# Performance work log

Hardware: AMD Instinct MI355X
Metric: run time of the kernel (lower is better)

Reference implementation:

```python
import jax, jax.numpy as jnp
import numpy as np

N = 50000
E = 800000
D_IN = 128
D_OUT = 64


def setup_inputs() -> dict:
    key = jax.random.key(0)
    ks = jax.random.split(key, 8)
    x = jax.random.normal(ks[0], (N, D_IN), dtype=jnp.float32)
    edge_index = jax.random.randint(ks[1], (2, E), 0, N, dtype=jnp.int64)
    s = 1.0 / np.sqrt(D_IN)
    # PyG SAGEConv: lin_l (applied to aggregated neighbors, has bias), lin_r (root, no bias)
    w1_l = jax.random.uniform(ks[2], (D_IN, D_IN), jnp.float32, -s, s)
    b1 = jnp.zeros((D_IN,), jnp.float32)
    w1_r = jax.random.uniform(ks[3], (D_IN, D_IN), jnp.float32, -s, s)
    w2_l = jax.random.uniform(ks[4], (D_IN, D_OUT), jnp.float32, -s, s)
    b2 = jnp.zeros((D_OUT,), jnp.float32)
    w2_r = jax.random.uniform(ks[5], (D_IN, D_OUT), jnp.float32, -s, s)
    return {"x": x, "edge_index": edge_index, "w1_l": w1_l, "b1": b1,
            "w1_r": w1_r, "w2_l": w2_l, "b2": b2, "w2_r": w2_r}


def _sage_conv(x, src, dst, w_l, b_l, w_r):
    # mean-aggregate source features at destination nodes
    msg_sum = jax.ops.segment_sum(x[src], dst, num_segments=N)  # [N, d]
    cnt = jax.ops.segment_sum(jnp.ones((src.shape[0],), x.dtype), dst, num_segments=N)
    mean = msg_sum / jnp.maximum(cnt, 1.0)[:, None]
    out = mean @ w_l + b_l + x @ w_r
    # L2 normalize (normalize=True)
    norm = jnp.linalg.norm(out, axis=-1, keepdims=True)
    return out / jnp.maximum(norm, 1e-12)


def reference(x, edge_index, w1_l, b1, w1_r, w2_l, b2, w2_r):
    src, dst = edge_index[0], edge_index[1]
    h = _sage_conv(x, src, dst, w1_l, b1, w1_r)
    h = _sage_conv(h, src, dst, w2_l, b2, w2_r)
    return h
```

## Files before the change

### kernel.cpp

```cpp
#include <hip/hip_runtime.h>
#include <math.h>

#define NN 50000
#define EE 800000
#define NB 196
#define CAP 6144

typedef __attribute__((ext_vector_type(8))) short bf16x8;
typedef __attribute__((ext_vector_type(16))) float f32x16;
typedef __attribute__((ext_vector_type(4))) unsigned short us4;

__device__ inline unsigned short bf16_rne(float f) {
    union { float f; unsigned u; } a; a.f = f;
    unsigned u = a.u;
    u += 0x7fff + ((u >> 16) & 1);
    return (unsigned short)(u >> 16);
}
__device__ inline float bf16_to_f32(unsigned short u) {
    union { unsigned u; float f; } a; a.u = ((unsigned)u) << 16;
    return a.f;
}

__global__ __launch_bounds__(1024) void bin_kernel(
        const int* __restrict__ src, const int* __restrict__ dst,
        int* __restrict__ gcur, int* __restrict__ rec, int E) {
    __shared__ int hist[NB];
    __shared__ int cur[NB];
    const int t = threadIdx.x;
    const int per = (E + gridDim.x - 1) / gridDim.x;
    const int lo = blockIdx.x * per;
    const int hi = min(lo + per, E);

    for (int i = t; i < NB; i += 1024) hist[i] = 0;
    __syncthreads();
    for (int e = lo + t; e < hi; e += 1024)
        atomicAdd(&hist[dst[e] >> 8], 1);
    __syncthreads();
    for (int i = t; i < NB; i += 1024)
        cur[i] = atomicAdd(&gcur[i], hist[i]);
    __syncthreads();
    for (int e = lo + t; e < hi; e += 1024) {
        int d = dst[e], s = src[e];
        int cb = d >> 8;
        int p = atomicAdd(&cur[cb], 1);
        if (p < CAP) rec[(size_t)cb * CAP + p] = ((d & 255) << 16) | s;
    }
}

__global__ __launch_bounds__(256) void bucket_deg_kernel(
        const int* __restrict__ rec, const int* __restrict__ bcur,
        int* __restrict__ deg, int n) {
    __shared__ int cnt[256];
    const int cb = blockIdx.x, t = threadIdx.x;
    cnt[t] = 0;
    __syncthreads();
    int m = bcur[cb]; if (m > CAP) m = CAP;
    const int* r = rec + (size_t)cb * CAP;
    for (int i = t; i < m; i += 256) atomicAdd(&cnt[r[i] >> 16], 1);
    __syncthreads();
    int node = cb * 256 + t;
    if (node < n) deg[node] = cnt[t];
}

__global__ void scan1_kernel(const int* __restrict__ deg, int* __restrict__ bsum, int n) {
    __shared__ int s[256];
    int t = threadIdx.x;
    int i = blockIdx.x * 256 + t;
    s[t] = (i < n) ? deg[i] : 0;
    __syncthreads();
    for (int ofs = 128; ofs > 0; ofs >>= 1) {
        if (t < ofs) s[t] += s[t + ofs];
        __syncthreads();
    }
    if (t == 0) bsum[blockIdx.x] = s[0];
}

__global__ void scan2_kernel(int* __restrict__ bsum, int nb) {
    __shared__ int s[256];
    int t = threadIdx.x;
    s[t] = (t < nb) ? bsum[t] : 0;
    __syncthreads();
    for (int ofs = 1; ofs < 256; ofs <<= 1) {
        int v = s[t];
        int a = (t >= ofs) ? s[t - ofs] : 0;
        __syncthreads();
        s[t] = v + a;
        __syncthreads();
    }
    if (t < nb) bsum[t] = (t == 0) ? 0 : s[t - 1];
}

__global__ void scan3_kernel(const int* __restrict__ deg, const int* __restrict__ bsum,
                             int* __restrict__ rowoff, int n) {
    __shared__ int s[256];
    int t = threadIdx.x;
    int i = blockIdx.x * 256 + t;
    int d = (i < n) ? deg[i] : 0;
    s[t] = d;
    __syncthreads();
    for (int ofs = 1; ofs < 256; ofs <<= 1) {
        int v = s[t];
        int a = (t >= ofs) ? s[t - ofs] : 0;
        __syncthreads();
        s[t] = v + a;
        __syncthreads();
    }
    int excl = s[t] - d + bsum[blockIdx.x];
    if (i < n) rowoff[i] = excl;
    if (i == n - 1) rowoff[n] = excl + d;
}

__global__ __launch_bounds__(256) void place_kernel(
        const int* __restrict__ rec, const int* __restrict__ bcur,
        const int* __restrict__ rowoff, unsigned short* __restrict__ csr, int n) {
    __shared__ int cnt[256];
    __shared__ int cur[256];
    __shared__ unsigned short sorted[CAP];
    const int cb = blockIdx.x, t = threadIdx.x;
    int m = bcur[cb]; if (m > CAP) m = CAP;
    const int* r = rec + (size_t)cb * CAP;

    cnt[t] = 0;
    __syncthreads();
    for (int i = t; i < m; i += 256) atomicAdd(&cnt[r[i] >> 16], 1);
    __syncthreads();
    int orig = cnt[t];
    for (int ofs = 1; ofs < 256; ofs <<= 1) {
        int v = cnt[t];
        int a = (t >= ofs) ? cnt[t - ofs] : 0;
        __syncthreads();
        cnt[t] = v + a;
        __syncthreads();
    }
    cur[t] = cnt[t] - orig;
    __syncthreads();
    for (int i = t; i < m; i += 256) {
        int rr = r[i];
        int pos = atomicAdd(&cur[rr >> 16], 1);
        sorted[pos] = (unsigned short)(rr & 0xffff);
    }
    __syncthreads();
    const int base = rowoff[cb * 256];
    for (int i = t; i < m; i += 256) csr[base + i] = sorted[i];
}

__global__ void prep_w_kernel(const float* __restrict__ wl, const float* __restrict__ wr,
                              unsigned short* __restrict__ wt, int HALF, int K) {
    int idx = blockIdx.x * 256 + threadIdx.x;
    int total = 2 * HALF * K;
    if (idx >= total) return;
    int n = idx / K, k = idx % K;
    float v = (n < HALF) ? wl[(size_t)k * HALF + n] : wr[(size_t)k * HALF + (n - HALF)];
    wt[idx] = bf16_rne(v);
}

template <int CO, bool BF16IN>
__global__ __launch_bounds__(256) void transform_mfma_kernel(
        const void* __restrict__ xin, const unsigned short* __restrict__ wt,
        const float* __restrict__ bias, unsigned short* __restrict__ ybuf,
        float* __restrict__ rbuf, int n) {
    constexpr int HALF = CO / 2;
    constexpr int LDW = 136;
    __shared__ unsigned short Xs[64][LDW];
    __shared__ unsigned short Ws[64][LDW];

    const int t = threadIdx.x;
    const int node0 = blockIdx.x * 64;
    const int gy = blockIdx.y;

    if (BF16IN) {
        const unsigned short* xb = (const unsigned short*)xin;
        for (int e = t; e < 64 * 16; e += 256) {
            int nd = e >> 4, c8 = e & 15;
            int node = node0 + nd;
            int4 v = (node < n) ? ((const int4*)(xb + (size_t)node * 128))[c8]
                                : make_int4(0, 0, 0, 0);
            *(int4*)&Xs[nd][c8 * 8] = v;
        }
    } else {
        const float* xf = (const float*)xin;
        for (int e = t; e < 64 * 32; e += 256) {
            int nd = e >> 5, c4 = e & 31;
            int node = node0 + nd;
            float4 v = (node < n) ? ((const float4*)xf)[(size_t)node * 32 + c4]
                                  : make_float4(0.f, 0.f, 0.f, 0.f);
            us4 p;
            p.x = bf16_rne(v.x); p.y = bf16_rne(v.y); p.z = bf16_rne(v.z); p.w = bf16_rne(v.w);
            *(us4*)&Xs[nd][c4 * 4] = p;
        }
    }
    for (int e = t; e < 64 * 16; e += 256) {
        int nd = e >> 4, c8 = e & 15;
        int4 v = ((const int4*)(wt + ((size_t)(gy * 64 + nd)) * 128))[c8];
        *(int4*)&Ws[nd][c8 * 8] = v;
    }
    __syncthreads();

    const int lane = t & 63, wave = t >> 6;
    const int wm = (wave & 1) * 32, wn = (wave >> 1) * 32;
    const int ml = wm + (lane & 31);
    const int nl = wn + (lane & 31);
    const int koff = (lane >> 5) * 8;

    f32x16 acc;
#pragma unroll
    for (int r = 0; r < 16; r++) acc[r] = 0.f;

#pragma unroll
    for (int kk = 0; kk < 8; kk++) {
        bf16x8 a = *(const bf16x8*)&Xs[ml][kk * 16 + koff];
        bf16x8 b = *(const bf16x8*)&Ws[nl][kk * 16 + koff];
        acc = __builtin_amdgcn_mfma_f32_32x32x16_bf16(a, b, acc, 0, 0, 0);
    }

    const int col = gy * 64 + wn + (lane & 31);
    if (col < HALF) {
#pragma unroll
        for (int r = 0; r < 16; r++) {
            int row = (r & 3) + 8 * (r >> 2) + 4 * (lane >> 5);
            int node = node0 + wm + row;
            if (node < n) ybuf[(size_t)node * HALF + col] = bf16_rne(acc[r]);
        }
    } else {
        const float bj = bias[col - HALF];
#pragma unroll
        for (int r = 0; r < 16; r++) {
            int row = (r & 3) + 8 * (r >> 2) + 4 * (lane >> 5);
            int node = node0 + wm + row;
            if (node < n) rbuf[(size_t)node * HALF + (col - HALF)] = acc[r] + bj;
        }
    }
}

template <bool OUTBF16>
__global__ __launch_bounds__(256) void gather128_kernel(
        const unsigned short* __restrict__ y, const float* __restrict__ rr,
        const int* __restrict__ rowoff, const unsigned short* __restrict__ csr,
        void* __restrict__ out, int n) {
    const int wave = threadIdx.x >> 6;
    const int lane = threadIdx.x & 63;
    const int node = blockIdx.x * 4 + wave;
    if (node >= n) return;

    const int off = rowoff[node];
    const int end = rowoff[node + 1];
    const int deg = end - off;

    float2 acc = make_float2(0.f, 0.f);
    for (int k0 = 0; k0 < deg; k0 += 8) {
        int idx[8];
#pragma unroll
        for (int i = 0; i < 8; i++) {
            int kk = off + k0 + i;
            idx[i] = csr[kk < end ? kk : end - 1];
        }
        unsigned v[8];
#pragma unroll
        for (int i = 0; i < 8; i++)
            v[i] = *(const unsigned*)(y + (size_t)idx[i] * 128 + 2 * lane);
#pragma unroll
        for (int i = 0; i < 8; i++)
            if (k0 + i < deg) {
                acc.x += bf16_to_f32((unsigned short)(v[i] & 0xffff));
                acc.y += bf16_to_f32((unsigned short)(v[i] >> 16));
            }
    }
    float im = 1.0f / fmaxf((float)deg, 1.0f);
    float2 rv = *(const float2*)(rr + (size_t)node * 128 + 2 * lane);
    float2 v = make_float2(acc.x * im + rv.x, acc.y * im + rv.y);
    float s = v.x * v.x + v.y * v.y;
#pragma unroll
    for (int m = 32; m >= 1; m >>= 1) s += __shfl_xor(s, m, 64);
    float rn = 1.0f / fmaxf(sqrtf(s), 1e-12f);
    v.x *= rn; v.y *= rn;
    if (OUTBF16) {
        unsigned pk = (unsigned)bf16_rne(v.x) | ((unsigned)bf16_rne(v.y) << 16);
        *(unsigned*)((unsigned short*)out + (size_t)node * 128 + 2 * lane) = pk;
    } else {
        *(float2*)((float*)out + (size_t)node * 128 + 2 * lane) = v;
    }
}

__global__ __launch_bounds__(256) void gather64_kernel(
        const unsigned short* __restrict__ y, const float* __restrict__ rr,
        const int* __restrict__ rowoff, const unsigned short* __restrict__ csr,
        float* __restrict__ out, int n) {
    const int wave = threadIdx.x >> 6;
    const int lane = threadIdx.x & 63;
    const int node = blockIdx.x * 4 + wave;
    if (node >= n) return;

    const int off = rowoff[node];
    const int end = rowoff[node + 1];
    const int deg = end - off;

    float acc = 0.f;
    for (int k0 = 0; k0 < deg; k0 += 8) {
        int idx[8];
#pragma unroll
        for (int i = 0; i < 8; i++) {
            int kk = off + k0 + i;
            idx[i] = csr[kk < end ? kk : end - 1];
        }
        unsigned short v[8];
#pragma unroll
        for (int i = 0; i < 8; i++)
            v[i] = y[(size_t)idx[i] * 64 + lane];
#pragma unroll
        for (int i = 0; i < 8; i++)
            if (k0 + i < deg) acc += bf16_to_f32(v[i]);
    }
    float im = 1.0f / fmaxf((float)deg, 1.0f);
    float r = rr[(size_t)node * 64 + lane];
    float v = acc * im + r;
    float s = v * v;
#pragma unroll
    for (int m = 32; m >= 1; m >>= 1) s += __shfl_xor(s, m, 64);
    float rn = 1.0f / fmaxf(sqrtf(s), 1e-12f);
    out[(size_t)node * 64 + lane] = v * rn;
}

extern "C" void kernel_launch(void* const* d_in, const int* in_sizes, int n_in,
                              void* d_out, int out_size, void* d_ws, size_t ws_size,
                              hipStream_t stream) {
    const float* x   = (const float*)d_in[0];
    const int*   ei  = (const int*)d_in[1];
    const float* w1l = (const float*)d_in[2];
    const float* b1  = (const float*)d_in[3];
    const float* w1r = (const float*)d_in[4];
    const float* w2l = (const float*)d_in[5];
    const float* b2  = (const float*)d_in[6];
    const float* w2r = (const float*)d_in[7];
    float* out = (float*)d_out;

    const int* src = ei;
    const int* dst = ei + EE;

    char* ws = (char*)d_ws;
    auto align = [](size_t v) { return (v + 255) & ~(size_t)255; };
    int*   deg    = (int*)ws;                 size_t o = align((size_t)NN * 4);
    int*   rowoff = (int*)(ws + o);           o += align((size_t)(NN + 1) * 4);
    int*   bcur   = (int*)(ws + o);           o += align((size_t)NB * 4);
    int*   bsum   = (int*)(ws + o);           o += align((size_t)NB * 4);
    int*   rec    = (int*)(ws + o);           o += align((size_t)NB * CAP * 4);
    unsigned short* csr = (unsigned short*)(ws + o); o += align((size_t)EE * 2);
    unsigned short* wt1 = (unsigned short*)(ws + o); o += align((size_t)256 * 128 * 2);
    unsigned short* wt2 = (unsigned short*)(ws + o); o += align((size_t)128 * 128 * 2);
    unsigned short* y1  = (unsigned short*)(ws + o); o += align((size_t)NN * 128 * 2);
    float*          r1  = (float*)(ws + o);          o += align((size_t)NN * 128 * 4);
    unsigned short* h1  = (unsigned short*)(ws + o); o += align((size_t)NN * 128 * 2);
    unsigned short* y2  = (unsigned short*)(ws + o); o += align((size_t)NN * 64 * 2);
    float*          r2  = (float*)(ws + o);          o += align((size_t)NN * 64 * 4);

    hipMemsetAsync(bcur, 0, (size_t)NB * 4, stream);
    bin_kernel<<<128, 1024, 0, stream>>>(src, dst, bcur, rec, EE);
    bucket_deg_kernel<<<NB, 256, 0, stream>>>(rec, bcur, deg, NN);
    scan1_kernel<<<NB, 256, 0, stream>>>(deg, bsum, NN);
    scan2_kernel<<<1, 256, 0, stream>>>(bsum, NB);
    scan3_kernel<<<NB, 256, 0, stream>>>(deg, bsum, rowoff, NN);
    place_kernel<<<NB, 256, 0, stream>>>(rec, bcur, rowoff, csr, NN);

    prep_w_kernel<<<(256 * 128 + 255) / 256, 256, 0, stream>>>(w1l, w1r, wt1, 128, 128);
    prep_w_kernel<<<(128 * 128 + 255) / 256, 256, 0, stream>>>(w2l, w2r, wt2, 64, 128);

    transform_mfma_kernel<256, false><<<dim3((NN + 63) / 64, 4), 256, 0, stream>>>(
        x, wt1, b1, y1, r1, NN);
    gather128_kernel<true><<<(NN + 3) / 4, 256, 0, stream>>>(y1, r1, rowoff, csr, h1, NN);

    transform_mfma_kernel<128, true><<<dim3((NN + 63) / 64, 2), 256, 0, stream>>>(
        h1, wt2, b2, y2, r2, NN);
    gather64_kernel<<<(NN + 3) / 4, 256, 0, stream>>>(y2, r2, rowoff, csr, out, NN);
}
```

Before: 227.1 us.

## Unroll gathers deeper, pad zero row, split 64-wide gather across half-waves, fuse scan1

The 128-wide gather now loads 16 neighbors per iteration instead of 8. Out-of-range slots point at a zero-filled padding row, which removes the per-element predicate from the accumulate loop. The 64-wide gather has each half-wave handle alternate edges with 4-byte loads, and the two halves are combined with a shuffle. The degree-count kernel also computes the per-bucket block sum, which drops one kernel launch. The cost is two extra small memsets and more registers per thread from the wider unroll.

```diff
diff --git a/kernel.cpp b/kernel.cpp
--- a/kernel.cpp
+++ b/kernel.cpp
@@ -16,8 +16,12 @@
     u += 0x7fff + ((u >> 16) & 1);
     return (unsigned short)(u >> 16);
 }
-__device__ inline float bf16_to_f32(unsigned short u) {
-    union { unsigned u; float f; } a; a.u = ((unsigned)u) << 16;
+__device__ inline float bf16_lo(unsigned v) {
+    union { unsigned u; float f; } a; a.u = v << 16;
+    return a.f;
+}
+__device__ inline float bf16_hi(unsigned v) {
+    union { unsigned u; float f; } a; a.u = v & 0xffff0000u;
     return a.f;
 }
 
@@ -47,9 +51,9 @@
     }
 }
 
-__global__ __launch_bounds__(256) void bucket_deg_kernel(
+__global__ __launch_bounds__(256) void bucket_deg_scan1_kernel(
         const int* __restrict__ rec, const int* __restrict__ bcur,
-        int* __restrict__ deg, int n) {
+        int* __restrict__ deg, int* __restrict__ bsum, int n) {
     __shared__ int cnt[256];
     const int cb = blockIdx.x, t = threadIdx.x;
     cnt[t] = 0;
@@ -59,20 +63,14 @@
     for (int i = t; i < m; i += 256) atomicAdd(&cnt[r[i] >> 16], 1);
     __syncthreads();
     int node = cb * 256 + t;
-    if (node < n) deg[node] = cnt[t];
-}
-
-__global__ void scan1_kernel(const int* __restrict__ deg, int* __restrict__ bsum, int n) {
-    __shared__ int s[256];
-    int t = threadIdx.x;
-    int i = blockIdx.x * 256 + t;
-    s[t] = (i < n) ? deg[i] : 0;
+    int d = cnt[t];
+    if (node < n) deg[node] = d;
     __syncthreads();
     for (int ofs = 128; ofs > 0; ofs >>= 1) {
-        if (t < ofs) s[t] += s[t + ofs];
-        __syncthreads();
-    }
-    if (t == 0) bsum[blockIdx.x] = s[0];
+        if (t < ofs) cnt[t] += cnt[t + ofs];
+        __syncthreads();
+    }
+    if (t == 0) bsum[cb] = cnt[0];
 }
 
 __global__ void scan2_kernel(int* __restrict__ bsum, int nb) {
@@ -247,23 +245,22 @@
     const int deg = end - off;
 
     float2 acc = make_float2(0.f, 0.f);
-    for (int k0 = 0; k0 < deg; k0 += 8) {
-        int idx[8];
-#pragma unroll
-        for (int i = 0; i < 8; i++) {
+    for (int k0 = 0; k0 < deg; k0 += 16) {
+        int idx[16];
+#pragma unroll
+        for (int i = 0; i < 16; i++) {
             int kk = off + k0 + i;
-            idx[i] = csr[kk < end ? kk : end - 1];
-        }
-        unsigned v[8];
-#pragma unroll
-        for (int i = 0; i < 8; i++)
+            idx[i] = (kk < end) ? (int)csr[kk] : n;
+        }
+        unsigned v[16];
+#pragma unroll
+        for (int i = 0; i < 16; i++)
             v[i] = *(const unsigned*)(y + (size_t)idx[i] * 128 + 2 * lane);
 #pragma unroll
-        for (int i = 0; i < 8; i++)
-            if (k0 + i < deg) {
-                acc.x += bf16_to_f32((unsigned short)(v[i] & 0xffff));
-                acc.y += bf16_to_f32((unsigned short)(v[i] >> 16));
-            }
+        for (int i = 0; i < 16; i++) {
+            acc.x += bf16_lo(v[i]);
+            acc.y += bf16_hi(v[i]);
+        }
     }
     float im = 1.0f / fmaxf((float)deg, 1.0f);
     float2 rv = *(const float2*)(rr + (size_t)node * 128 + 2 * lane);
@@ -289,35 +286,45 @@
     const int lane = threadIdx.x & 63;
     const int node = blockIdx.x * 4 + wave;
     if (node >= n) return;
+    const int half = lane >> 5;
+    const int l32 = lane & 31;
 
     const int off = rowoff[node];
     const int end = rowoff[node + 1];
     const int deg = end - off;
-
-    float acc = 0.f;
-    for (int k0 = 0; k0 < deg; k0 += 8) {
+    const int P = (deg + 1) >> 1;
+
+    float2 acc = make_float2(0.f, 0.f);
+    for (int p0 = 0; p0 < P; p0 += 8) {
         int idx[8];
 #pragma unroll
         for (int i = 0; i < 8; i++) {
-            int kk = off + k0 + i;
-            idx[i] = csr[kk < end ? kk : end - 1];
-        }
-        unsigned short v[8];
+            int kk = off + 2 * (p0 + i) + half;
+            idx[i] = (kk < end) ? (int)csr[kk] : n;
+        }
+        unsigned v[8];
 #pragma unroll
         for (int i = 0; i < 8; i++)
-            v[i] = y[(size_t)idx[i] * 64 + lane];
-#pragma unroll
-        for (int i = 0; i < 8; i++)
-            if (k0 + i < deg) acc += bf16_to_f32(v[i]);
-    }
+            v[i] = *(const unsigned*)(y + (size_t)idx[i] * 64 + 2 * l32);
+#pragma unroll
+        for (int i = 0; i < 8; i++) {
+            acc.x += bf16_lo(v[i]);
+            acc.y += bf16_hi(v[i]);
+        }
+    }
+    acc.x += __shfl_xor(acc.x, 32, 64);
+    acc.y += __shfl_xor(acc.y, 32, 64);
+
     float im = 1.0f / fmaxf((float)deg, 1.0f);
-    float r = rr[(size_t)node * 64 + lane];
-    float v = acc * im + r;
-    float s = v * v;
+    float2 rv = *(const float2*)(rr + (size_t)node * 64 + 2 * l32);
+    float2 v = make_float2(acc.x * im + rv.x, acc.y * im + rv.y);
+    float s = v.x * v.x + v.y * v.y;
 #pragma unroll
     for (int m = 32; m >= 1; m >>= 1) s += __shfl_xor(s, m, 64);
+    s *= 0.5f;
     float rn = 1.0f / fmaxf(sqrtf(s), 1e-12f);
-    out[(size_t)node * 64 + lane] = v * rn;
+    if (half == 0)
+        *(float2*)(out + (size_t)node * 64 + 2 * l32) = make_float2(v.x * rn, v.y * rn);
 }
 
 extern "C" void kernel_launch(void* const* d_in, const int* in_sizes, int n_in,
@@ -346,16 +353,17 @@
     unsigned short* csr = (unsigned short*)(ws + o); o += align((size_t)EE * 2);
     unsigned short* wt1 = (unsigned short*)(ws + o); o += align((size_t)256 * 128 * 2);
     unsigned short* wt2 = (unsigned short*)(ws + o); o += align((size_t)128 * 128 * 2);
-    unsigned short* y1  = (unsigned short*)(ws + o); o += align((size_t)NN * 128 * 2);
+    unsigned short* y1  = (unsigned short*)(ws + o); o += align((size_t)(NN + 1) * 128 * 2);
     float*          r1  = (float*)(ws + o);          o += align((size_t)NN * 128 * 4);
     unsigned short* h1  = (unsigned short*)(ws + o); o += align((size_t)NN * 128 * 2);
-    unsigned short* y2  = (unsigned short*)(ws + o); o += align((size_t)NN * 64 * 2);
+    unsigned short* y2  = (unsigned short*)(ws + o); o += align((size_t)(NN + 1) * 64 * 2);
     float*          r2  = (float*)(ws + o);          o += align((size_t)NN * 64 * 4);
 
     hipMemsetAsync(bcur, 0, (size_t)NB * 4, stream);
+    hipMemsetAsync(y1 + (size_t)NN * 128, 0, 256, stream);
+    hipMemsetAsync(y2 + (size_t)NN * 64, 0, 128, stream);
     bin_kernel<<<128, 1024, 0, stream>>>(src, dst, bcur, rec, EE);
-    bucket_deg_kernel<<<NB, 256, 0, stream>>>(rec, bcur, deg, NN);
-    scan1_kernel<<<NB, 256, 0, stream>>>(deg, bsum, NN);
+    bucket_deg_scan1_kernel<<<NB, 256, 0, stream>>>(rec, bcur, deg, bsum, NN);
     scan2_kernel<<<1, 256, 0, stream>>>(bsum, NB);
     scan3_kernel<<<NB, 256, 0, stream>>>(deg, bsum, rowoff, NN);
     place_kernel<<<NB, 256, 0, stream>>>(rec, bcur, rowoff, csr, NN);
```

After: 220.5 us. -2.9%, faster.
